# Kernel tuning notes

Hardware: AMD Instinct MI355X
Metric: run time of the kernel (lower is better)

The kernel has to match this reference:

```python
import jax, jax.numpy as jnp
import numpy as np

NUM_NODES = 50000
NUM_EDGES = 800000
IN_DIM = 128
OUT_DIM = 128


def setup_inputs() -> dict:
    key = jax.random.key(0)
    k1, k2, k3 = jax.random.split(key, 3)
    x = jax.random.normal(k1, (NUM_NODES, IN_DIM), dtype=jnp.float32)
    edge_index = jax.random.randint(k2, (2, NUM_EDGES), 0, NUM_NODES, dtype=jnp.int64)
    # xavier_uniform-like init
    limit = float(np.sqrt(6.0 / (IN_DIM + OUT_DIM)))
    weight = jax.random.uniform(k3, (IN_DIM, OUT_DIM), minval=-limit, maxval=limit, dtype=jnp.float32)
    bias = jnp.zeros((OUT_DIM,), dtype=jnp.float32)
    return {"x": x, "edge_index": edge_index, "weight": weight, "bias": bias}


def reference(x, edge_index, weight, bias):
    num_nodes = x.shape[0]
    # add self loops
    self_loops = jnp.broadcast_to(jnp.arange(num_nodes, dtype=edge_index.dtype)[None, :], (2, num_nodes))
    ei = jnp.concatenate([edge_index, self_loops], axis=1)  # [2, E+N]
    row, col = ei[0], ei[1]

    transformed = x @ weight  # [N, out_dim]

    # symmetric normalization: deg counted over source indices (row), as in original
    deg = jax.ops.segment_sum(jnp.ones_like(row, dtype=x.dtype), row, num_segments=num_nodes)
    deg_inv_sqrt = jnp.where(deg > 0, deg ** -0.5, 0.0)
    norm = deg_inv_sqrt[row] * deg_inv_sqrt[col]  # [E+N]

    # gather-scale-scatter: out[dst] += norm * transformed[src]
    messages = norm[:, None] * transformed[row]  # [E+N, out_dim]
    out = jax.ops.segment_sum(messages, col, num_segments=num_nodes)
    return out + bias
```

## Files before the change

### kernel.cpp

```cpp
#include <hip/hip_runtime.h>
#include <hip/hip_fp16.h>


#define EPB 4096

typedef _Float16 f16;
typedef f16 f16x8 __attribute__((ext_vector_type(8)));
typedef float f32x4 __attribute__((ext_vector_type(4)));

static inline int cdiv(int a, int b) { return (a + b - 1) / b; }

__global__ __launch_bounds__(256) void k_hist(const int* __restrict__ ei, int E,
                                              int* __restrict__ hist, int nblk, int nbins) {
  __shared__ int ha[256], hb[256];
  const int tid = threadIdx.x, blk = blockIdx.x;
  ha[tid] = 0; hb[tid] = 0;
  __syncthreads();
  const int base = blk * EPB;
  for (int i = tid; i < EPB; i += 256) {
    int e = base + i;
    if (e >= E) break;
    int src = ei[e];
    int dst = ei[E + e];
    atomicAdd(&ha[dst >> 8], 1);
    atomicAdd(&hb[src >> 8], 1);
  }
  __syncthreads();
  if (tid < nbins) {
    hist[tid * nblk + blk] = ha[tid];
    hist[nbins * nblk + tid * nblk + blk] = hb[tid];
  }
}

__global__ __launch_bounds__(256) void k_scan1(int* __restrict__ a,
                                               int* __restrict__ partials, int M) {
  __shared__ int ws[256];
  const int tid = threadIdx.x;
  const int i0 = blockIdx.x * 1024 + tid * 4;
  int v0 = (i0 + 0 < M) ? a[i0 + 0] : 0;
  int v1 = (i0 + 1 < M) ? a[i0 + 1] : 0;
  int v2 = (i0 + 2 < M) ? a[i0 + 2] : 0;
  int v3 = (i0 + 3 < M) ? a[i0 + 3] : 0;
  int tsum = v0 + v1 + v2 + v3;
  ws[tid] = tsum;
  __syncthreads();
#pragma unroll
  for (int off = 1; off < 256; off <<= 1) {
    int add = (tid >= off) ? ws[tid - off] : 0;
    __syncthreads();
    ws[tid] += add;
    __syncthreads();
  }
  int texcl = ws[tid] - tsum;
  if (tid == 255) partials[blockIdx.x] = ws[255];
  if (i0 + 0 < M) a[i0 + 0] = texcl;
  if (i0 + 1 < M) a[i0 + 1] = texcl + v0;
  if (i0 + 2 < M) a[i0 + 2] = texcl + v0 + v1;
  if (i0 + 3 < M) a[i0 + 3] = texcl + v0 + v1 + v2;
}

__global__ __launch_bounds__(256) void k_scan2(int* __restrict__ p, int nb) {
  __shared__ int ws[256];
  const int tid = threadIdx.x;
  int v = (tid < nb) ? p[tid] : 0;
  ws[tid] = v;
  __syncthreads();
#pragma unroll
  for (int off = 1; off < 256; off <<= 1) {
    int add = (tid >= off) ? ws[tid - off] : 0;
    __syncthreads();
    ws[tid] += add;
    __syncthreads();
  }
  if (tid < nb) p[tid] = ws[tid] - v;
}

__global__ __launch_bounds__(256) void k_wt(const float* __restrict__ W,
                                            f16* __restrict__ WhT) {
  int gid = blockIdx.x * 256 + threadIdx.x;
  int k = gid >> 7, c = gid & 127;
  WhT[c * 128 + k] = (f16)W[gid];
}

__global__ __launch_bounds__(256) void k_part(const int* __restrict__ ei, int E,
                                              const int* __restrict__ hist,
                                              const int* __restrict__ partials,
                                              int nblk, int nbins,
                                              int* __restrict__ ebA,
                                              unsigned char* __restrict__ ebB) {
  __shared__ int cA[256], cB[256];
  const int tid = threadIdx.x, blk = blockIdx.x;
  const int HALF = nbins * nblk;
  if (tid < nbins) {
    int ia = tid * nblk + blk;
    int ib = HALF + tid * nblk + blk;
    cA[tid] = hist[ia] + partials[ia >> 10];
    cB[tid] = hist[ib] + partials[ib >> 10] - E;
  }
  __syncthreads();
  const int base = blk * EPB;
  for (int i = tid; i < EPB; i += 256) {
    int e = base + i;
    if (e >= E) break;
    int src = ei[e];
    int dst = ei[E + e];
    int pa = atomicAdd(&cA[dst >> 8], 1);
    ebA[pa] = (src << 8) | (dst & 255);
    int pb = atomicAdd(&cB[src >> 8], 1);
    ebB[pb] = (unsigned char)(src & 255);
  }
}

__global__ __launch_bounds__(256) void k_deg(const unsigned char* __restrict__ ebB,
                                             const int* __restrict__ hist,
                                             const int* __restrict__ partials,
                                             int nblk, int nbins, int E,
                                             float* __restrict__ dis, int N) {
  __shared__ int h[256];
  const int tid = threadIdx.x, b = blockIdx.x;
  const int HALF = nbins * nblk;
  int i0 = HALF + b * nblk;
  const int bs = hist[i0] + partials[i0 >> 10] - E;
  int be = E;
  if (b + 1 < nbins) {
    int i1 = HALF + (b + 1) * nblk;
    be = hist[i1] + partials[i1 >> 10] - E;
  }
  h[tid] = 0;
  __syncthreads();
  for (int j = bs + tid; j < be; j += 256) atomicAdd(&h[ebB[j]], 1);
  __syncthreads();
  int node = b * 256 + tid;
  if (node < N) dis[node] = rsqrtf(1.0f + (float)h[tid]);
}

__global__ __launch_bounds__(256) void k_csr(const int* __restrict__ ebA,
                                             const int* __restrict__ hist,
                                             const int* __restrict__ partials,
                                             int nblk, int nbins, int E,
                                             int* __restrict__ offs,
                                             int* __restrict__ srcs, int N) {
  __shared__ int h[256], tmp[256], cur[256];
  const int tid = threadIdx.x, b = blockIdx.x;
  int i0 = b * nblk;
  const int bs = hist[i0] + partials[i0 >> 10];
  int be = E;
  if (b + 1 < nbins) {
    int i1 = (b + 1) * nblk;
    be = hist[i1] + partials[i1 >> 10];
  }
  h[tid] = 0;
  __syncthreads();
  for (int j = bs + tid; j < be; j += 256) atomicAdd(&h[ebA[j] & 255], 1);
  __syncthreads();
  int cnt = h[tid];
  tmp[tid] = cnt;
  __syncthreads();
#pragma unroll
  for (int off = 1; off < 256; off <<= 1) {
    int add = (tid >= off) ? tmp[tid - off] : 0;
    __syncthreads();
    tmp[tid] += add;
    __syncthreads();
  }
  int gpos = bs + tmp[tid] - cnt;
  int node = b * 256 + tid;
  if (node < N) offs[node] = gpos;
  cur[tid] = gpos;
  __syncthreads();
  for (int j = bs + tid; j < be; j += 256) {
    int v = ebA[j];
    int p = atomicAdd(&cur[v & 255], 1);
    srcs[p] = v >> 8;
  }
  if (b == 0 && tid == 0) offs[N] = E;
}

__global__ __launch_bounds__(256) void k_gemm_mfma(
    const float* __restrict__ x, const f16* __restrict__ WhT,
    const float* __restrict__ dis, __half* __restrict__ t2h, int N) {
  __shared__ __align__(16) f16 cs[4][16][136];
  const int tid = threadIdx.x;
  const int w = tid >> 6, l = tid & 63;
  const int l15 = l & 15, lg = l >> 4;
  const int wr0 = blockIdx.x * 64 + w * 16;
  const int arow = wr0 + l15;
  const bool avalid = arow < N;

  f32x4 acc[8];
#pragma unroll
  for (int ct = 0; ct < 8; ++ct) acc[ct] = (f32x4){0.f, 0.f, 0.f, 0.f};

#pragma unroll
  for (int kc = 0; kc < 4; ++kc) {
    f16x8 af;
    if (avalid) {
      const float4* ap = (const float4*)(x + (size_t)arow * 128 + kc * 32 + lg * 8);
      float4 a0 = ap[0], a1 = ap[1];
      af[0] = (f16)a0.x; af[1] = (f16)a0.y; af[2] = (f16)a0.z; af[3] = (f16)a0.w;
      af[4] = (f16)a1.x; af[5] = (f16)a1.y; af[6] = (f16)a1.z; af[7] = (f16)a1.w;
    } else {
#pragma unroll
      for (int j = 0; j < 8; ++j) af[j] = (f16)0.f;
    }
#pragma unroll
    for (int ct = 0; ct < 8; ++ct) {
      f16x8 bf = *(const f16x8*)(WhT + (ct * 16 + l15) * 128 + kc * 32 + lg * 8);
      acc[ct] = __builtin_amdgcn_mfma_f32_16x16x32_f16(af, bf, acc[ct], 0, 0, 0);
    }
  }

  float d4[4];
#pragma unroll
  for (int j = 0; j < 4; ++j) {
    int r = wr0 + lg * 4 + j;
    d4[j] = (r < N) ? dis[r] : 0.f;
  }
#pragma unroll
  for (int ct = 0; ct < 8; ++ct)
#pragma unroll
    for (int j = 0; j < 4; ++j)
      cs[w][lg * 4 + j][ct * 16 + l15] = (f16)(d4[j] * acc[ct][j]);
  __syncthreads();

#pragma unroll
  for (int it = 0; it < 4; ++it) {
    int t = it * 64 + l;
    int row = t >> 4, seg = t & 15;
    int gr = wr0 + row;
    if (gr < N)
      *(f16x8*)((f16*)t2h + (size_t)gr * 128 + seg * 8) = *(const f16x8*)&cs[w][row][seg * 8];
  }
}

__global__ __launch_bounds__(256) void k_gather(
    const int* __restrict__ offs, const int* __restrict__ srcs,
    const __half* __restrict__ t2h, const float* __restrict__ dis,
    const float* __restrict__ bias, float* __restrict__ out, int N) {
  const int node = blockIdx.x * 4 + (threadIdx.x >> 6);
  const int lane = threadIdx.x & 63;
  if (node >= N) return;

  const int s = offs[node];
  const int e = offs[node + 1];
  const __half2* t2h2 = (const __half2*)t2h;

  float2 acc = __half22float2(t2h2[(size_t)node * 64 + lane]);
  int j = s;
  for (; j + 3 < e; j += 4) {
    int s0 = srcs[j], s1 = srcs[j + 1], s2 = srcs[j + 2], s3 = srcs[j + 3];
    float2 v0 = __half22float2(t2h2[(size_t)s0 * 64 + lane]);
    float2 v1 = __half22float2(t2h2[(size_t)s1 * 64 + lane]);
    float2 v2 = __half22float2(t2h2[(size_t)s2 * 64 + lane]);
    float2 v3 = __half22float2(t2h2[(size_t)s3 * 64 + lane]);
    acc.x += (v0.x + v1.x) + (v2.x + v3.x);
    acc.y += (v0.y + v1.y) + (v2.y + v3.y);
  }
  for (; j < e; ++j) {
    float2 v = __half22float2(t2h2[(size_t)srcs[j] * 64 + lane]);
    acc.x += v.x;
    acc.y += v.y;
  }

  const float dn = dis[node];
  const float2 b = *(const float2*)(bias + (size_t)lane * 2);
  float2 r = make_float2(dn * acc.x + b.x, dn * acc.y + b.y);
  *(float2*)(out + (size_t)node * 128 + (size_t)lane * 2) = r;
}

extern "C" void kernel_launch(void* const* d_in, const int* in_sizes, int n_in,
                              void* d_out, int out_size, void* d_ws, size_t ws_size,
                              hipStream_t stream) {
  const float* x = (const float*)d_in[0];
  const int* ei = (const int*)d_in[1];
  const float* W = (const float*)d_in[2];
  const float* bias = (const float*)d_in[3];
  float* out = (float*)d_out;

  const int N = in_sizes[0] / 128;
  const int E = in_sizes[1] / 2;
  const int NBLK = cdiv(E, EPB);
  const int NBINS = cdiv(N, 256);
  const int M = 2 * NBINS * NBLK;
  const int NB1 = cdiv(M, 1024);

  __half* t2h = (__half*)d_ws;
  int* hist = (int*)d_ws;
  int* partials = hist + M;
  int* ebA = partials + 256;
  unsigned char* ebB = (unsigned char*)(ebA + E);
  float* dis = (float*)(t2h + (size_t)N * 128);
  int* offs = (int*)(dis + N);
  int* srcs = offs + (N + 1);
  f16* WhT = (f16*)(srcs + E);

  k_hist<<<NBLK, 256, 0, stream>>>(ei, E, hist, NBLK, NBINS);
  k_scan1<<<NB1, 256, 0, stream>>>(hist, partials, M);
  k_scan2<<<1, 256, 0, stream>>>(partials, NB1);
  k_wt<<<64, 256, 0, stream>>>(W, WhT);
  k_part<<<NBLK, 256, 0, stream>>>(ei, E, hist, partials, NBLK, NBINS, ebA, ebB);
  k_deg<<<NBINS, 256, 0, stream>>>(ebB, hist, partials, NBLK, NBINS, E, dis, N);
  k_csr<<<NBINS, 256, 0, stream>>>(ebA, hist, partials, NBLK, NBINS, E, offs, srcs, N);
  k_gemm_mfma<<<cdiv(N, 64), 256, 0, stream>>>(x, WhT, dis, t2h, N);
  k_gather<<<cdiv(N, 4), 256, 0, stream>>>(offs, srcs, t2h, dis, bias, out, N);
}
```

Measured before the change: 112.0 us.

## Merge setup kernels and split gather wavefront into two half-waves over edges

The W transpose is folded into the single-block scan2 kernel, and the degree and CSR-build kernels are merged into one bucket kernel, which removes two launches. The gather kernel now has each half-wavefront handle alternate edges, loading 8-byte f16x4 chunks per lane, then combines the two halves with a cross-lane shuffle. This doubles the independent row loads in flight per wave and cuts launch overhead. In exchange the one-block scan kernel serially does the whole 16K-element transpose, and half the lanes sit idle during the final write.

```diff
diff --git a/kernel.cpp b/kernel.cpp
--- a/kernel.cpp
+++ b/kernel.cpp
@@ -5,6 +5,7 @@
 #define EPB 4096
 
 typedef _Float16 f16;
+typedef f16 f16x4 __attribute__((ext_vector_type(4)));
 typedef f16 f16x8 __attribute__((ext_vector_type(8)));
 typedef float f32x4 __attribute__((ext_vector_type(4)));
 
@@ -59,7 +60,9 @@
   if (i0 + 3 < M) a[i0 + 3] = texcl + v0 + v1 + v2;
 }
 
-__global__ __launch_bounds__(256) void k_scan2(int* __restrict__ p, int nb) {
+__global__ __launch_bounds__(256) void k_scan2wt(int* __restrict__ p, int nb,
+                                                 const float* __restrict__ W,
+                                                 f16* __restrict__ WhT) {
   __shared__ int ws[256];
   const int tid = threadIdx.x;
   int v = (tid < nb) ? p[tid] : 0;
@@ -73,13 +76,11 @@
     __syncthreads();
   }
   if (tid < nb) p[tid] = ws[tid] - v;
-}
-
-__global__ __launch_bounds__(256) void k_wt(const float* __restrict__ W,
-                                            f16* __restrict__ WhT) {
-  int gid = blockIdx.x * 256 + threadIdx.x;
-  int k = gid >> 7, c = gid & 127;
-  WhT[c * 128 + k] = (f16)W[gid];
+#pragma unroll 4
+  for (int i = tid; i < 128 * 128; i += 256) {
+    int k = i >> 7, c = i & 127;
+    WhT[c * 128 + k] = (f16)W[i];
+  }
 }
 
 __global__ __launch_bounds__(256) void k_part(const int* __restrict__ ei, int E,
@@ -111,69 +112,66 @@
   }
 }
 
-__global__ __launch_bounds__(256) void k_deg(const unsigned char* __restrict__ ebB,
-                                             const int* __restrict__ hist,
-                                             const int* __restrict__ partials,
-                                             int nblk, int nbins, int E,
-                                             float* __restrict__ dis, int N) {
-  __shared__ int h[256];
+__global__ __launch_bounds__(256) void k_bucket(
+    const int* __restrict__ ebA, const unsigned char* __restrict__ ebB,
+    const int* __restrict__ hist, const int* __restrict__ partials,
+    int nblk, int nbins, int E,
+    float* __restrict__ dis, int* __restrict__ offs,
+    int* __restrict__ srcs, int N) {
+  __shared__ int h[256], tmp[256], cur[256];
   const int tid = threadIdx.x, b = blockIdx.x;
   const int HALF = nbins * nblk;
-  int i0 = HALF + b * nblk;
-  const int bs = hist[i0] + partials[i0 >> 10] - E;
-  int be = E;
-  if (b + 1 < nbins) {
-    int i1 = HALF + (b + 1) * nblk;
-    be = hist[i1] + partials[i1 >> 10] - E;
-  }
-  h[tid] = 0;
-  __syncthreads();
-  for (int j = bs + tid; j < be; j += 256) atomicAdd(&h[ebB[j]], 1);
-  __syncthreads();
-  int node = b * 256 + tid;
-  if (node < N) dis[node] = rsqrtf(1.0f + (float)h[tid]);
-}
-
-__global__ __launch_bounds__(256) void k_csr(const int* __restrict__ ebA,
-                                             const int* __restrict__ hist,
-                                             const int* __restrict__ partials,
-                                             int nblk, int nbins, int E,
-                                             int* __restrict__ offs,
-                                             int* __restrict__ srcs, int N) {
-  __shared__ int h[256], tmp[256], cur[256];
-  const int tid = threadIdx.x, b = blockIdx.x;
-  int i0 = b * nblk;
-  const int bs = hist[i0] + partials[i0 >> 10];
-  int be = E;
-  if (b + 1 < nbins) {
-    int i1 = (b + 1) * nblk;
-    be = hist[i1] + partials[i1 >> 10];
-  }
-  h[tid] = 0;
-  __syncthreads();
-  for (int j = bs + tid; j < be; j += 256) atomicAdd(&h[ebA[j] & 255], 1);
-  __syncthreads();
-  int cnt = h[tid];
-  tmp[tid] = cnt;
-  __syncthreads();
-#pragma unroll
-  for (int off = 1; off < 256; off <<= 1) {
-    int add = (tid >= off) ? tmp[tid - off] : 0;
-    __syncthreads();
-    tmp[tid] += add;
-    __syncthreads();
-  }
-  int gpos = bs + tmp[tid] - cnt;
-  int node = b * 256 + tid;
-  if (node < N) offs[node] = gpos;
-  cur[tid] = gpos;
-  __syncthreads();
-  for (int j = bs + tid; j < be; j += 256) {
-    int v = ebA[j];
-    int p = atomicAdd(&cur[v & 255], 1);
-    srcs[p] = v >> 8;
-  }
-  if (b == 0 && tid == 0) offs[N] = E;
+  const int node = b * 256 + tid;
+
+  {
+    int i0 = HALF + b * nblk;
+    const int bs = hist[i0] + partials[i0 >> 10] - E;
+    int be = E;
+    if (b + 1 < nbins) {
+      int i1 = HALF + (b + 1) * nblk;
+      be = hist[i1] + partials[i1 >> 10] - E;
+    }
+    h[tid] = 0;
+    __syncthreads();
+    for (int j = bs + tid; j < be; j += 256) atomicAdd(&h[ebB[j]], 1);
+    __syncthreads();
+    if (node < N) dis[node] = rsqrtf(1.0f + (float)h[tid]);
+    __syncthreads();
+  }
+
+  {
+    int i0 = b * nblk;
+    const int bs = hist[i0] + partials[i0 >> 10];
+    int be = E;
+    if (b + 1 < nbins) {
+      int i1 = (b + 1) * nblk;
+      be = hist[i1] + partials[i1 >> 10];
+    }
+    h[tid] = 0;
+    __syncthreads();
+    for (int j = bs + tid; j < be; j += 256) atomicAdd(&h[ebA[j] & 255], 1);
+    __syncthreads();
+    int cnt = h[tid];
+    tmp[tid] = cnt;
+    __syncthreads();
+#pragma unroll
+    for (int off = 1; off < 256; off <<= 1) {
+      int add = (tid >= off) ? tmp[tid - off] : 0;
+      __syncthreads();
+      tmp[tid] += add;
+      __syncthreads();
+    }
+    int gpos = bs + tmp[tid] - cnt;
+    if (node < N) offs[node] = gpos;
+    cur[tid] = gpos;
+    __syncthreads();
+    for (int j = bs + tid; j < be; j += 256) {
+      int v = ebA[j];
+      int p = atomicAdd(&cur[v & 255], 1);
+      srcs[p] = v >> 8;
+    }
+    if (b == 0 && tid == 0) offs[N] = E;
+  }
 }
 
 __global__ __launch_bounds__(256) void k_gemm_mfma(
@@ -238,34 +236,53 @@
     const __half* __restrict__ t2h, const float* __restrict__ dis,
     const float* __restrict__ bias, float* __restrict__ out, int N) {
   const int node = blockIdx.x * 4 + (threadIdx.x >> 6);
-  const int lane = threadIdx.x & 63;
+  const int l = threadIdx.x & 63;
   if (node >= N) return;
+  const int half = l >> 5, sl = l & 31;
 
   const int s = offs[node];
   const int e = offs[node + 1];
-  const __half2* t2h2 = (const __half2*)t2h;
-
-  float2 acc = __half22float2(t2h2[(size_t)node * 64 + lane]);
-  int j = s;
-  for (; j + 3 < e; j += 4) {
-    int s0 = srcs[j], s1 = srcs[j + 1], s2 = srcs[j + 2], s3 = srcs[j + 3];
-    float2 v0 = __half22float2(t2h2[(size_t)s0 * 64 + lane]);
-    float2 v1 = __half22float2(t2h2[(size_t)s1 * 64 + lane]);
-    float2 v2 = __half22float2(t2h2[(size_t)s2 * 64 + lane]);
-    float2 v3 = __half22float2(t2h2[(size_t)s3 * 64 + lane]);
-    acc.x += (v0.x + v1.x) + (v2.x + v3.x);
-    acc.y += (v0.y + v1.y) + (v2.y + v3.y);
-  }
-  for (; j < e; ++j) {
-    float2 v = __half22float2(t2h2[(size_t)srcs[j] * 64 + lane]);
-    acc.x += v.x;
-    acc.y += v.y;
-  }
-
-  const float dn = dis[node];
-  const float2 b = *(const float2*)(bias + (size_t)lane * 2);
-  float2 r = make_float2(dn * acc.x + b.x, dn * acc.y + b.y);
-  *(float2*)(out + (size_t)node * 128 + (size_t)lane * 2) = r;
+  const f16x4* t2v = (const f16x4*)t2h;
+
+  float4 acc = make_float4(0.f, 0.f, 0.f, 0.f);
+  if (half == 0) {
+    f16x4 v = t2v[(size_t)node * 32 + sl];
+    acc.x = (float)v[0]; acc.y = (float)v[1]; acc.z = (float)v[2]; acc.w = (float)v[3];
+  }
+
+  int j = s + half;
+  for (; j + 6 < e; j += 8) {
+    int s0 = srcs[j], s1 = srcs[j + 2], s2 = srcs[j + 4], s3 = srcs[j + 6];
+    f16x4 v0 = t2v[(size_t)s0 * 32 + sl];
+    f16x4 v1 = t2v[(size_t)s1 * 32 + sl];
+    f16x4 v2 = t2v[(size_t)s2 * 32 + sl];
+    f16x4 v3 = t2v[(size_t)s3 * 32 + sl];
+    acc.x += ((float)v0[0] + (float)v1[0]) + ((float)v2[0] + (float)v3[0]);
+    acc.y += ((float)v0[1] + (float)v1[1]) + ((float)v2[1] + (float)v3[1]);
+    acc.z += ((float)v0[2] + (float)v1[2]) + ((float)v2[2] + (float)v3[2]);
+    acc.w += ((float)v0[3] + (float)v1[3]) + ((float)v2[3] + (float)v3[3]);
+  }
+  for (; j < e; j += 2) {
+    f16x4 v = t2v[(size_t)srcs[j] * 32 + sl];
+    acc.x += (float)v[0]; acc.y += (float)v[1];
+    acc.z += (float)v[2]; acc.w += (float)v[3];
+  }
+
+  acc.x += __shfl_xor(acc.x, 32);
+  acc.y += __shfl_xor(acc.y, 32);
+  acc.z += __shfl_xor(acc.z, 32);
+  acc.w += __shfl_xor(acc.w, 32);
+
+  if (half == 0) {
+    const float dn = dis[node];
+    const float4 b = ((const float4*)bias)[sl];
+    float4 r;
+    r.x = dn * acc.x + b.x;
+    r.y = dn * acc.y + b.y;
+    r.z = dn * acc.z + b.z;
+    r.w = dn * acc.w + b.w;
+    ((float4*)(out + (size_t)node * 128))[sl] = r;
+  }
 }
 
 extern "C" void kernel_launch(void* const* d_in, const int* in_sizes, int n_in,
@@ -296,11 +313,10 @@
 
   k_hist<<<NBLK, 256, 0, stream>>>(ei, E, hist, NBLK, NBINS);
   k_scan1<<<NB1, 256, 0, stream>>>(hist, partials, M);
-  k_scan2<<<1, 256, 0, stream>>>(partials, NB1);
-  k_wt<<<64, 256, 0, stream>>>(W, WhT);
+  k_scan2wt<<<1, 256, 0, stream>>>(partials, NB1, W, WhT);
   k_part<<<NBLK, 256, 0, stream>>>(ei, E, hist, partials, NBLK, NBINS, ebA, ebB);
-  k_deg<<<NBINS, 256, 0, stream>>>(ebB, hist, partials, NBLK, NBINS, E, dis, N);
-  k_csr<<<NBINS, 256, 0, stream>>>(ebA, hist, partials, NBLK, NBINS, E, offs, srcs, N);
+  k_bucket<<<NBINS, 256, 0, stream>>>(ebA, ebB, hist, partials, NBLK, NBINS, E,
+                                      dis, offs, srcs, N);
   k_gemm_mfma<<<cdiv(N, 64), 256, 0, stream>>>(x, WhT, dis, t2h, N);
   k_gather<<<cdiv(N, 4), 256, 0, stream>>>(offs, srcs, t2h, dis, bias, out, N);
 }
```

Result: slower. 118.8 us (+6.0%).

## Fuse CSR build kernels into one persistent kernel with grid barriers

Applied to the files above, without the earlier changes.

Merges the histogram, two scan stages, weight transpose, partition, degree and CSR kernels into a single persistent launch separated by atomic grid-wide barriers. Edge indices are cached in shared memory between the histogram and partition phases, so they are not re-read from global memory. This removes several kernel launch gaps and one edge reload. In exchange it relies on all blocks being co-resident, since the spin barrier would deadlock otherwise, and it adds a memset for the barrier counter.

```diff
diff --git a/kernel.cpp b/kernel.cpp
--- a/kernel.cpp
+++ b/kernel.cpp
@@ -10,170 +10,163 @@
 
 static inline int cdiv(int a, int b) { return (a + b - 1) / b; }
 
-__global__ __launch_bounds__(256) void k_hist(const int* __restrict__ ei, int E,
-                                              int* __restrict__ hist, int nblk, int nbins) {
-  __shared__ int ha[256], hb[256];
-  const int tid = threadIdx.x, blk = blockIdx.x;
-  ha[tid] = 0; hb[tid] = 0;
+__device__ __forceinline__ void grid_bar(int* cnt, int target, int tid) {
   __syncthreads();
-  const int base = blk * EPB;
-  for (int i = tid; i < EPB; i += 256) {
-    int e = base + i;
-    if (e >= E) break;
-    int src = ei[e];
-    int dst = ei[E + e];
-    atomicAdd(&ha[dst >> 8], 1);
-    atomicAdd(&hb[src >> 8], 1);
+  if (tid == 0) {
+    __threadfence();
+    __hip_atomic_fetch_add(cnt, 1, __ATOMIC_RELEASE, __HIP_MEMORY_SCOPE_AGENT);
+    while (__hip_atomic_load(cnt, __ATOMIC_ACQUIRE, __HIP_MEMORY_SCOPE_AGENT) < target) {}
   }
   __syncthreads();
-  if (tid < nbins) {
-    hist[tid * nblk + blk] = ha[tid];
-    hist[nbins * nblk + tid * nblk + blk] = hb[tid];
-  }
-}
-
-__global__ __launch_bounds__(256) void k_scan1(int* __restrict__ a,
-                                               int* __restrict__ partials, int M) {
-  __shared__ int ws[256];
-  const int tid = threadIdx.x;
-  const int i0 = blockIdx.x * 1024 + tid * 4;
-  int v0 = (i0 + 0 < M) ? a[i0 + 0] : 0;
-  int v1 = (i0 + 1 < M) ? a[i0 + 1] : 0;
-  int v2 = (i0 + 2 < M) ? a[i0 + 2] : 0;
-  int v3 = (i0 + 3 < M) ? a[i0 + 3] : 0;
-  int tsum = v0 + v1 + v2 + v3;
-  ws[tid] = tsum;
-  __syncthreads();
-#pragma unroll
-  for (int off = 1; off < 256; off <<= 1) {
-    int add = (tid >= off) ? ws[tid - off] : 0;
-    __syncthreads();
-    ws[tid] += add;
-    __syncthreads();
-  }
-  int texcl = ws[tid] - tsum;
-  if (tid == 255) partials[blockIdx.x] = ws[255];
-  if (i0 + 0 < M) a[i0 + 0] = texcl;
-  if (i0 + 1 < M) a[i0 + 1] = texcl + v0;
-  if (i0 + 2 < M) a[i0 + 2] = texcl + v0 + v1;
-  if (i0 + 3 < M) a[i0 + 3] = texcl + v0 + v1 + v2;
-}
-
-__global__ __launch_bounds__(256) void k_scan2(int* __restrict__ p, int nb) {
-  __shared__ int ws[256];
-  const int tid = threadIdx.x;
-  int v = (tid < nb) ? p[tid] : 0;
-  ws[tid] = v;
-  __syncthreads();
-#pragma unroll
-  for (int off = 1; off < 256; off <<= 1) {
-    int add = (tid >= off) ? ws[tid - off] : 0;
-    __syncthreads();
-    ws[tid] += add;
-    __syncthreads();
-  }
-  if (tid < nb) p[tid] = ws[tid] - v;
-}
-
-__global__ __launch_bounds__(256) void k_wt(const float* __restrict__ W,
-                                            f16* __restrict__ WhT) {
-  int gid = blockIdx.x * 256 + threadIdx.x;
-  int k = gid >> 7, c = gid & 127;
-  WhT[c * 128 + k] = (f16)W[gid];
-}
-
-__global__ __launch_bounds__(256) void k_part(const int* __restrict__ ei, int E,
-                                              const int* __restrict__ hist,
-                                              const int* __restrict__ partials,
-                                              int nblk, int nbins,
-                                              int* __restrict__ ebA,
-                                              unsigned char* __restrict__ ebB) {
-  __shared__ int cA[256], cB[256];
+}
+
+__global__ __launch_bounds__(256) void k_build(
+    const int* __restrict__ ei, int E, int N,
+    int nblk, int nbins, int nb1, int NG,
+    int* __restrict__ hist, int* __restrict__ partials,
+    int* __restrict__ ebA, unsigned char* __restrict__ ebB,
+    float* __restrict__ dis, int* __restrict__ offs, int* __restrict__ srcs,
+    const float* __restrict__ W, f16* __restrict__ WhT, int* cnt) {
+  __shared__ int esrc[EPB], edst[EPB];
+  __shared__ int shA[256], shB[256], shC[256];
   const int tid = threadIdx.x, blk = blockIdx.x;
   const int HALF = nbins * nblk;
-  if (tid < nbins) {
-    int ia = tid * nblk + blk;
-    int ib = HALF + tid * nblk + blk;
-    cA[tid] = hist[ia] + partials[ia >> 10];
-    cB[tid] = hist[ib] + partials[ib >> 10] - E;
-  }
-  __syncthreads();
-  const int base = blk * EPB;
-  for (int i = tid; i < EPB; i += 256) {
-    int e = base + i;
-    if (e >= E) break;
-    int src = ei[e];
-    int dst = ei[E + e];
-    int pa = atomicAdd(&cA[dst >> 8], 1);
-    ebA[pa] = (src << 8) | (dst & 255);
-    int pb = atomicAdd(&cB[src >> 8], 1);
-    ebB[pb] = (unsigned char)(src & 255);
-  }
-}
-
-__global__ __launch_bounds__(256) void k_deg(const unsigned char* __restrict__ ebB,
-                                             const int* __restrict__ hist,
-                                             const int* __restrict__ partials,
-                                             int nblk, int nbins, int E,
-                                             float* __restrict__ dis, int N) {
-  __shared__ int h[256];
-  const int tid = threadIdx.x, b = blockIdx.x;
-  const int HALF = nbins * nblk;
-  int i0 = HALF + b * nblk;
-  const int bs = hist[i0] + partials[i0 >> 10] - E;
-  int be = E;
-  if (b + 1 < nbins) {
-    int i1 = HALF + (b + 1) * nblk;
-    be = hist[i1] + partials[i1 >> 10] - E;
-  }
-  h[tid] = 0;
-  __syncthreads();
-  for (int j = bs + tid; j < be; j += 256) atomicAdd(&h[ebB[j]], 1);
-  __syncthreads();
-  int node = b * 256 + tid;
-  if (node < N) dis[node] = rsqrtf(1.0f + (float)h[tid]);
-}
-
-__global__ __launch_bounds__(256) void k_csr(const int* __restrict__ ebA,
-                                             const int* __restrict__ hist,
-                                             const int* __restrict__ partials,
-                                             int nblk, int nbins, int E,
-                                             int* __restrict__ offs,
-                                             int* __restrict__ srcs, int N) {
-  __shared__ int h[256], tmp[256], cur[256];
-  const int tid = threadIdx.x, b = blockIdx.x;
-  int i0 = b * nblk;
-  const int bs = hist[i0] + partials[i0 >> 10];
-  int be = E;
-  if (b + 1 < nbins) {
-    int i1 = (b + 1) * nblk;
-    be = hist[i1] + partials[i1 >> 10];
-  }
-  h[tid] = 0;
-  __syncthreads();
-  for (int j = bs + tid; j < be; j += 256) atomicAdd(&h[ebA[j] & 255], 1);
-  __syncthreads();
-  int cnt = h[tid];
-  tmp[tid] = cnt;
-  __syncthreads();
-#pragma unroll
-  for (int off = 1; off < 256; off <<= 1) {
-    int add = (tid >= off) ? tmp[tid - off] : 0;
-    __syncthreads();
-    tmp[tid] += add;
-    __syncthreads();
-  }
-  int gpos = bs + tmp[tid] - cnt;
-  int node = b * 256 + tid;
-  if (node < N) offs[node] = gpos;
-  cur[tid] = gpos;
-  __syncthreads();
-  for (int j = bs + tid; j < be; j += 256) {
-    int v = ebA[j];
-    int p = atomicAdd(&cur[v & 255], 1);
-    srcs[p] = v >> 8;
-  }
-  if (b == 0 && tid == 0) offs[N] = E;
+
+  if (blk < nblk) {
+    shA[tid] = 0; shB[tid] = 0;
+    __syncthreads();
+    const int base = blk * EPB;
+    const int lim = min(EPB, E - base);
+    for (int i = tid; i < lim; i += 256) {
+      int s = ei[base + i], d = ei[E + base + i];
+      esrc[i] = s; edst[i] = d;
+      atomicAdd(&shA[d >> 8], 1);
+      atomicAdd(&shB[s >> 8], 1);
+    }
+    __syncthreads();
+    if (tid < nbins) {
+      hist[tid * nblk + blk] = shA[tid];
+      hist[HALF + tid * nblk + blk] = shB[tid];
+    }
+  }
+  grid_bar(cnt, NG, tid);
+
+  if (blk < nb1) {
+    const int M = 2 * HALF;
+    const int i0 = blk * 1024 + tid * 4;
+    int v0 = (i0 + 0 < M) ? hist[i0 + 0] : 0;
+    int v1 = (i0 + 1 < M) ? hist[i0 + 1] : 0;
+    int v2 = (i0 + 2 < M) ? hist[i0 + 2] : 0;
+    int v3 = (i0 + 3 < M) ? hist[i0 + 3] : 0;
+    int tsum = v0 + v1 + v2 + v3;
+    shA[tid] = tsum;
+    __syncthreads();
+#pragma unroll
+    for (int off = 1; off < 256; off <<= 1) {
+      int add = (tid >= off) ? shA[tid - off] : 0;
+      __syncthreads();
+      shA[tid] += add;
+      __syncthreads();
+    }
+    int texcl = shA[tid] - tsum;
+    if (tid == 255) partials[blk] = shA[255];
+    if (i0 + 0 < M) hist[i0 + 0] = texcl;
+    if (i0 + 1 < M) hist[i0 + 1] = texcl + v0;
+    if (i0 + 2 < M) hist[i0 + 2] = texcl + v0 + v1;
+    if (i0 + 3 < M) hist[i0 + 3] = texcl + v0 + v1 + v2;
+  } else if (blk < nb1 + 64) {
+    int i = (blk - nb1) * 256 + tid;
+    int k = i >> 7, c = i & 127;
+    WhT[c * 128 + k] = (f16)W[i];
+  }
+  grid_bar(cnt, 2 * NG, tid);
+
+  if (blk == 0) {
+    int v = (tid < nb1) ? partials[tid] : 0;
+    shA[tid] = v;
+    __syncthreads();
+#pragma unroll
+    for (int off = 1; off < 256; off <<= 1) {
+      int add = (tid >= off) ? shA[tid - off] : 0;
+      __syncthreads();
+      shA[tid] += add;
+      __syncthreads();
+    }
+    if (tid < nb1) partials[tid] = shA[tid] - v;
+  }
+  grid_bar(cnt, 3 * NG, tid);
+
+  if (blk < nblk) {
+    if (tid < nbins) {
+      int ia = tid * nblk + blk;
+      int ib = HALF + tid * nblk + blk;
+      shA[tid] = hist[ia] + partials[ia >> 10];
+      shB[tid] = hist[ib] + partials[ib >> 10] - E;
+    }
+    __syncthreads();
+    const int base = blk * EPB;
+    const int lim = min(EPB, E - base);
+    for (int i = tid; i < lim; i += 256) {
+      int s = esrc[i], d = edst[i];
+      int pa = atomicAdd(&shA[d >> 8], 1);
+      ebA[pa] = (s << 8) | (d & 255);
+      int pb = atomicAdd(&shB[s >> 8], 1);
+      ebB[pb] = (unsigned char)(s & 255);
+    }
+  }
+  grid_bar(cnt, 4 * NG, tid);
+
+  if (blk < nbins) {
+    const int node = blk * 256 + tid;
+    {
+      int i0 = HALF + blk * nblk;
+      const int bs = hist[i0] + partials[i0 >> 10] - E;
+      int be = E;
+      if (blk + 1 < nbins) {
+        int i1 = HALF + (blk + 1) * nblk;
+        be = hist[i1] + partials[i1 >> 10] - E;
+      }
+      shA[tid] = 0;
+      __syncthreads();
+      for (int j = bs + tid; j < be; j += 256) atomicAdd(&shA[ebB[j]], 1);
+      __syncthreads();
+      if (node < N) dis[node] = rsqrtf(1.0f + (float)shA[tid]);
+      __syncthreads();
+    }
+    {
+      int i0 = blk * nblk;
+      const int bs = hist[i0] + partials[i0 >> 10];
+      int be = E;
+      if (blk + 1 < nbins) {
+        int i1 = (blk + 1) * nblk;
+        be = hist[i1] + partials[i1 >> 10];
+      }
+      shA[tid] = 0;
+      __syncthreads();
+      for (int j = bs + tid; j < be; j += 256) atomicAdd(&shA[ebA[j] & 255], 1);
+      __syncthreads();
+      int cnt_ = shA[tid];
+      shB[tid] = cnt_;
+      __syncthreads();
+#pragma unroll
+      for (int off = 1; off < 256; off <<= 1) {
+        int add = (tid >= off) ? shB[tid - off] : 0;
+        __syncthreads();
+        shB[tid] += add;
+        __syncthreads();
+      }
+      int gpos = bs + shB[tid] - cnt_;
+      if (node < N) offs[node] = gpos;
+      shC[tid] = gpos;
+      __syncthreads();
+      for (int j = bs + tid; j < be; j += 256) {
+        int v = ebA[j];
+        int p = atomicAdd(&shC[v & 255], 1);
+        srcs[p] = v >> 8;
+      }
+      if (blk == 0 && tid == 0) offs[N] = E;
+    }
+  }
 }
 
 __global__ __launch_bounds__(256) void k_gemm_mfma(
@@ -283,6 +276,8 @@
   const int NBINS = cdiv(N, 256);
   const int M = 2 * NBINS * NBLK;
   const int NB1 = cdiv(M, 1024);
+  int NG = NBLK > NBINS ? NBLK : NBINS;
+  if (NB1 + 64 > NG) NG = NB1 + 64;
 
   __half* t2h = (__half*)d_ws;
   int* hist = (int*)d_ws;
@@ -293,14 +288,12 @@
   int* offs = (int*)(dis + N);
   int* srcs = offs + (N + 1);
   f16* WhT = (f16*)(srcs + E);
-
-  k_hist<<<NBLK, 256, 0, stream>>>(ei, E, hist, NBLK, NBINS);
-  k_scan1<<<NB1, 256, 0, stream>>>(hist, partials, M);
-  k_scan2<<<1, 256, 0, stream>>>(partials, NB1);
-  k_wt<<<64, 256, 0, stream>>>(W, WhT);
-  k_part<<<NBLK, 256, 0, stream>>>(ei, E, hist, partials, NBLK, NBINS, ebA, ebB);
-  k_deg<<<NBINS, 256, 0, stream>>>(ebB, hist, partials, NBLK, NBINS, E, dis, N);
-  k_csr<<<NBINS, 256, 0, stream>>>(ebA, hist, partials, NBLK, NBINS, E, offs, srcs, N);
+  int* cnt = (int*)(WhT + 128 * 128);
+
+  hipMemsetAsync(cnt, 0, sizeof(int), stream);
+  k_build<<<NG, 256, 0, stream>>>(ei, E, N, NBLK, NBINS, NB1, NG,
+                                  hist, partials, ebA, ebB, dis, offs, srcs,
+                                  W, WhT, cnt);
   k_gemm_mfma<<<cdiv(N, 64), 256, 0, stream>>>(x, WhT, dis, t2h, N);
   k_gather<<<cdiv(N, 4), 256, 0, stream>>>(offs, srcs, t2h, dis, bias, out, N);
 }
```

Result: slower. 185.1 us (+65.3%).
